# Kernel optimization log

Hardware: AMD Instinct MI355X
Metric: run time of the kernel (lower is better)

The kernel has to match this reference:

```python
import jax, jax.numpy as jnp
import numpy as np
import math

NUM_GROUPS = 32
EPS = 1e-5

def group_norm(x, weight, bias):
    # x: (b, c, h, w); normalize over (c/G, h, w) within each group
    b, c, h, w = x.shape
    xg = x.reshape(b, NUM_GROUPS, c // NUM_GROUPS, h, w)
    mean = xg.mean(axis=(2, 3, 4), keepdims=True)
    var = xg.var(axis=(2, 3, 4), keepdims=True)
    xg = (xg - mean) * jax.lax.rsqrt(var + EPS)
    xn = xg.reshape(b, c, h, w)
    return xn * weight[None, :, None, None] + bias[None, :, None, None]


def setup_inputs() -> dict:
    key = jax.random.key(0)
    ks = jax.random.split(key, 3)
    b, c, h, w = 8, 256, 64, 64
    x = jax.random.normal(ks[0], (b, c, h, w), dtype=jnp.float32)
    gn_weight = jnp.ones((c,), dtype=jnp.float32)
    gn_bias = jnp.zeros((c,), dtype=jnp.float32)
    qkv_w = jax.random.normal(ks[1], (3 * c, c), dtype=jnp.float32) * (1.0 / math.sqrt(c))
    qkv_b = jnp.zeros((3 * c,), dtype=jnp.float32)
    out_w = jax.random.normal(ks[2], (c, c), dtype=jnp.float32) * (1.0 / math.sqrt(c))
    out_b = jnp.zeros((c,), dtype=jnp.float32)
    return {"x": x, "gn_weight": gn_weight, "gn_bias": gn_bias,
            "qkv_w": qkv_w, "qkv_b": qkv_b, "out_w": out_w, "out_b": out_b}


def reference(x, gn_weight, gn_bias, qkv_w, qkv_b, out_w, out_b):
    b, c, h, w = x.shape
    xn = group_norm(x, gn_weight, gn_bias)
    # 1x1 conv == per-pixel matmul: (3c, c) x (b, c, h, w) -> (b, 3c, h, w)
    qkv = jnp.einsum('oc,bchw->bohw', qkv_w, xn) + qkv_b[None, :, None, None]
    q, k, v = jnp.split(qkv, 3, axis=1)
    hw = h * w
    q = q.transpose(0, 2, 3, 1).reshape(b, hw, c)   # (b, hw, c)
    k = k.reshape(b, c, hw)                          # (b, c, hw)
    v = v.transpose(0, 2, 3, 1).reshape(b, hw, c)   # (b, hw, c)
    scale = 1.0 / math.sqrt(c)
    attn = jax.nn.softmax(jnp.einsum('bic,bcj->bij', q, k) * scale, axis=-1)
    out = jnp.einsum('bij,bjc->bic', attn, v)        # (b, hw, c)
    out = out.reshape(b, h, w, c).transpose(0, 3, 1, 2)  # (b, c, h, w)
    out = jnp.einsum('oc,bchw->bohw', out_w, out) + out_b[None, :, None, None]
    return out + x
```

## Files before the change

### kernel.cpp

```cpp
#include <hip/hip_runtime.h>

#define HW 4096
#define NC 256
#define NB 8
#define GN_EPS 1e-5f

typedef short bf16x8 __attribute__((ext_vector_type(8)));
typedef float f32x4 __attribute__((ext_vector_type(4)));
typedef float f32x16 __attribute__((ext_vector_type(16)));

#define MFMA16 __builtin_amdgcn_mfma_f32_16x16x32_bf16
#define MFMA32 __builtin_amdgcn_mfma_f32_32x32x16_bf16

#define SWZ(row) ((((row) & 7) ^ (((row) >> 3) & 7)) << 4)

#define QSCALE 0.09016844f

__device__ __forceinline__ unsigned short f2bf(float f) {
  unsigned int u = __float_as_uint(f);
  u = (u + 0x7FFFu + ((u >> 16) & 1u)) >> 16;
  return (unsigned short)u;
}
__device__ __forceinline__ float bf2f(unsigned short h) {
  return __uint_as_float(((unsigned int)h) << 16);
}

__device__ __forceinline__ void gload16(const void* g, void* l) {
  __builtin_amdgcn_global_load_lds(
      (const __attribute__((address_space(1))) void*)g,
      (__attribute__((address_space(3))) void*)l, 16, 0, 0);
}

__global__ void gn_stats_kernel(const float* __restrict__ x,
                                const float* __restrict__ gnw,
                                const float* __restrict__ gnb,
                                float* __restrict__ s_arr,
                                float* __restrict__ t_arr) {
  int bg = blockIdx.x;
  int b = bg >> 5, g = bg & 31;
  const float4* base = (const float4*)(x + ((size_t)b * NC + g * 8) * HW);
  int tid = threadIdx.x;
  float s = 0.f, ss = 0.f;
  for (int it = 0; it < 32; ++it) {
    float4 v = base[tid + it * 256];
    s += v.x + v.y + v.z + v.w;
    ss += v.x * v.x + v.y * v.y + v.z * v.z + v.w * v.w;
  }
  for (int off = 32; off; off >>= 1) {
    s += __shfl_down(s, off);
    ss += __shfl_down(ss, off);
  }
  __shared__ float red[8];
  __shared__ float bc[2];
  int wave = tid >> 6, lane = tid & 63;
  if (lane == 0) { red[wave] = s; red[4 + wave] = ss; }
  __syncthreads();
  if (tid == 0) {
    float S = red[0] + red[1] + red[2] + red[3];
    float SS = red[4] + red[5] + red[6] + red[7];
    float mean = S * (1.f / 32768.f);
    float var = SS * (1.f / 32768.f) - mean * mean;
    bc[0] = mean;
    bc[1] = rsqrtf(var + GN_EPS);
  }
  __syncthreads();
  if (tid < 8) {
    int c = g * 8 + tid;
    float sv = bc[1] * gnw[c];
    s_arr[b * NC + c] = sv;
    t_arr[b * NC + c] = gnb[c] - bc[0] * sv;
  }
}

__global__ __launch_bounds__(256) void qkv_gemm_kernel(
    const float* __restrict__ x, const float* __restrict__ s_arr,
    const float* __restrict__ t_arr, const float* __restrict__ w,
    const float* __restrict__ bias, unsigned short* __restrict__ qb,
    unsigned short* __restrict__ kc_, unsigned short* __restrict__ vc) {
  int b = blockIdx.z;
  int p0 = blockIdx.x * 64;
  int o0 = blockIdx.y * 128;
  int tid = threadIdx.x;
  int wave = tid >> 6, lane = tid & 63;
  int l15 = lane & 15, q4 = lane >> 4;
  int wm = wave >> 1, wn = wave & 1;
  __shared__ unsigned short a_lds[64 * 64];
  __shared__ unsigned short b_lds[128 * 64];
  char* aB = (char*)a_lds;
  char* bB = (char*)b_lds;
  f32x4 acc[2][4];
  for (int i = 0; i < 2; ++i)
    for (int j = 0; j < 4; ++j) acc[i][j] = (f32x4){0.f, 0.f, 0.f, 0.f};

  for (int kc0 = 0; kc0 < 256; kc0 += 64) {
    __syncthreads();
    for (int it = 0; it < 4; ++it) {
      int idx = tid + it * 256;
      int c = idx >> 4, p4 = idx & 15;
      float4 xv = *(const float4*)(x + ((size_t)b * NC + kc0 + c) * HW + p0 + p4 * 4);
      float sc = s_arr[b * NC + kc0 + c];
      float tc = t_arr[b * NC + kc0 + c];
      float vals[4] = {xv.x, xv.y, xv.z, xv.w};
      for (int i = 0; i < 4; ++i) {
        int p = p4 * 4 + i;
        *(unsigned short*)(aB + ((p * 128 + c * 2) ^ SWZ(p))) =
            f2bf(vals[i] * sc + tc);
      }
    }
    for (int it = 0; it < 8; ++it) {
      int idx = tid + it * 256;
      int o = idx >> 4, c4 = idx & 15;
      float4 wv = *(const float4*)(w + (size_t)(o0 + o) * NC + kc0 + c4 * 4);
      ushort4 hv = make_ushort4(f2bf(wv.x), f2bf(wv.y), f2bf(wv.z), f2bf(wv.w));
      *(ushort4*)(bB + ((o * 128 + c4 * 8) ^ SWZ(o))) = hv;
    }
    __syncthreads();
    for (int kk = 0; kk < 2; ++kk) {
      bf16x8 af[2], bfv[4];
      for (int pb = 0; pb < 2; ++pb) {
        int row = wm * 32 + pb * 16 + l15;
        af[pb] = *(const bf16x8*)(aB + ((row * 128 + kk * 64 + q4 * 16) ^ SWZ(row)));
      }
      for (int ob = 0; ob < 4; ++ob) {
        int row = wn * 64 + ob * 16 + l15;
        bfv[ob] = *(const bf16x8*)(bB + ((row * 128 + kk * 64 + q4 * 16) ^ SWZ(row)));
      }
      for (int pb = 0; pb < 2; ++pb)
        for (int ob = 0; ob < 4; ++ob)
          acc[pb][ob] = MFMA16(af[pb], bfv[ob], acc[pb][ob], 0, 0, 0);
    }
  }
  for (int pb = 0; pb < 2; ++pb) {
    for (int ob = 0; ob < 4; ++ob) {
      int og = o0 + wn * 64 + ob * 16 + l15;
      int tsel = og >> 8, oc = og & 255;
      float bi = bias[og];
      if (tsel == 2) {
        int p = p0 + wm * 32 + pb * 16 + q4 * 4;
        ushort4 pk4 = make_ushort4(
            f2bf(acc[pb][ob][0] + bi), f2bf(acc[pb][ob][1] + bi),
            f2bf(acc[pb][ob][2] + bi), f2bf(acc[pb][ob][3] + bi));
        *(ushort4*)(vc + (((size_t)b * 512 + (p >> 3)) * 256 + oc) * 8 + (p & 7)) =
            pk4;
      } else {
        for (int r = 0; r < 4; ++r) {
          int p = p0 + wm * 32 + pb * 16 + q4 * 4 + r;
          float val = acc[pb][ob][r] + bi;
          if (tsel == 0) {
            qb[((size_t)b * HW + p) * NC + oc] = f2bf(val * QSCALE);
          } else {
            kc_[((size_t)(b * 32 + (oc >> 3)) * HW + p) * 8 + (oc & 7)] = f2bf(val);
          }
        }
      }
    }
  }
}

__global__ __launch_bounds__(256, 2) void flash_attn_kernel(
    const unsigned short* __restrict__ qb, const unsigned short* __restrict__ kc_,
    const unsigned short* __restrict__ vc, unsigned short* __restrict__ Oh0,
    unsigned short* __restrict__ Oh1, float* __restrict__ Lb) {
  int b = blockIdx.x & 7;
  int qt = (blockIdx.x >> 3) & 31;
  int half = blockIdx.x >> 8;
  int tid = threadIdx.x;
  int wave = tid >> 6, lane = tid & 63;
  int l31 = lane & 31;
  int hi = lane >> 5;

  __shared__ unsigned short k_lds[2][8192];
  __shared__ unsigned short v_lds[2][8192];

  int j0b = half * 2048;

  const char* kp[4];
  const char* vp[4];
  {
    const char* kcb = (const char*)(kc_ + (size_t)b * 32 * HW * 8);
    const char* vcb = (const char*)(vc + (size_t)b * 512 * NC * 8);
#pragma unroll
    for (int i = 0; i < 4; ++i) {
      kp[i] = kcb + (size_t)((tid >> 5) + i * 8) * 65536 +
              (size_t)(j0b + (tid & 31)) * 16;
      vp[i] = vcb + (size_t)((j0b >> 3) + i) * 4096 + tid * 16;
    }
  }

  bf16x8 qf[16];
  {
    const unsigned short* qrow =
        qb + ((size_t)b * HW + qt * 128 + wave * 32 + l31) * NC;
#pragma unroll
    for (int kb = 0; kb < 16; ++kb)
      qf[kb] = *(const bf16x8*)(qrow + kb * 16 + hi * 8);
  }

  f32x16 acc[8];
#pragma unroll
  for (int nb = 0; nb < 8; ++nb)
#pragma unroll
    for (int i = 0; i < 16; ++i) acc[nb][i] = 0.f;
  float m_r = -1e30f, l_r = 0.f;

#pragma unroll
  for (int i = 0; i < 4; ++i)
    gload16(kp[i], (char*)k_lds[0] + tid * 16 + i * 4096);
#pragma unroll
  for (int i = 0; i < 4; ++i)
    gload16(vp[i], (char*)v_lds[0] + tid * 16 + i * 4096);
  __syncthreads();

  for (int t = 0; t < 64; ++t) {
    int cur = t & 1;
    if (t < 63) {
#pragma unroll
      for (int i = 0; i < 4; ++i) {
        kp[i] += 512;
        gload16(kp[i], (char*)k_lds[cur ^ 1] + tid * 16 + i * 4096);
      }
#pragma unroll
      for (int i = 0; i < 4; ++i) {
        vp[i] += 16384;
        gload16(vp[i], (char*)v_lds[cur ^ 1] + tid * 16 + i * 4096);
      }
    }
    const char* kB = (const char*)k_lds[cur];
    const char* vB = (const char*)v_lds[cur];

    f32x16 p;
#pragma unroll
    for (int i = 0; i < 16; ++i) p[i] = 0.f;
    __builtin_amdgcn_s_setprio(1);
#pragma unroll
    for (int kb = 0; kb < 16; ++kb) {
      bf16x8 kf = *(const bf16x8*)(kB + (kb * 2 + hi) * 512 + l31 * 16);
      p = MFMA32(kf, qf[kb], p, 0, 0, 0);
    }
    __builtin_amdgcn_s_setprio(0);

    float pmax;
    {
      float t0 = fmaxf(p[0], p[1]), t1 = fmaxf(p[2], p[3]);
      float t2 = fmaxf(p[4], p[5]), t3 = fmaxf(p[6], p[7]);
      float t4 = fmaxf(p[8], p[9]), t5 = fmaxf(p[10], p[11]);
      float t6 = fmaxf(p[12], p[13]), t7 = fmaxf(p[14], p[15]);
      float u0 = fmaxf(t0, t1), u1 = fmaxf(t2, t3);
      float u2 = fmaxf(t4, t5), u3 = fmaxf(t6, t7);
      pmax = fmaxf(fmaxf(u0, u1), fmaxf(u2, u3));
    }
    pmax = fmaxf(pmax, __shfl_xor(pmax, 32));
    if (!__all(pmax - m_r <= 12.0f)) {
      float mn = fmaxf(m_r, pmax);
      float sf = exp2f(m_r - mn);
      m_r = mn;
      l_r *= sf;
#pragma unroll
      for (int reg = 0; reg < 16; ++reg) {
        float sfr = __shfl(sf, (reg & 3) + 8 * (reg >> 2) + 4 * hi);
#pragma unroll
        for (int nb = 0; nb < 8; ++nb) acc[nb][reg] *= sfr;
      }
    }
#pragma unroll
    for (int i = 0; i < 16; ++i) p[i] = __builtin_amdgcn_exp2f(p[i] - m_r);
    float rs;
    {
      float t0 = p[0] + p[1], t1 = p[2] + p[3];
      float t2 = p[4] + p[5], t3 = p[6] + p[7];
      float t4 = p[8] + p[9], t5 = p[10] + p[11];
      float t6 = p[12] + p[13], t7 = p[14] + p[15];
      float u0 = t0 + t1, u1 = t2 + t3, u2 = t4 + t5, u3 = t6 + t7;
      rs = (u0 + u1) + (u2 + u3);
    }
    rs += __shfl_xor(rs, 32);
    l_r += rs;

    int pk[8];
#pragma unroll
    for (int i = 0; i < 8; ++i) {
      int r;
      asm("v_cvt_pk_bf16_f32 %0, %1, %2"
          : "=v"(r)
          : "v"(p[2 * i]), "v"(p[2 * i + 1]));
      pk[i] = r;
    }
    union PU { int w[4]; bf16x8 v; } pu[2];
#pragma unroll
    for (int kb = 0; kb < 2; ++kb) {
      int base = 4 * kb;
      int pushA = hi ? pk[base + 0] : pk[base + 2];
      int pushB = hi ? pk[base + 1] : pk[base + 3];
      int shA = __shfl_xor(pushA, 32);
      int shB = __shfl_xor(pushB, 32);
      pu[kb].w[0] = hi ? shA : pk[base + 0];
      pu[kb].w[1] = hi ? shB : pk[base + 1];
      pu[kb].w[2] = hi ? pk[base + 2] : shA;
      pu[kb].w[3] = hi ? pk[base + 3] : shB;
    }

    __builtin_amdgcn_s_setprio(1);
#pragma unroll
    for (int nb = 0; nb < 8; ++nb) {
#pragma unroll
      for (int kb = 0; kb < 2; ++kb) {
        bf16x8 vf = *(const bf16x8*)(vB + (kb * 2 + hi) * 4096 +
                                     (nb * 32 + l31) * 16);
        acc[nb] = MFMA32(pu[kb].v, vf, acc[nb], 0, 0, 0);
      }
    }
    __builtin_amdgcn_s_setprio(0);
    __syncthreads();
  }

  float linv = 1.f / l_r;
  unsigned short* Ohp = (half ? Oh1 : Oh0) +
                        ((size_t)b * HW + qt * 128 + wave * 32) * NC;
#pragma unroll
  for (int reg = 0; reg < 16; ++reg) {
    int row = (reg & 3) + 8 * (reg >> 2) + 4 * hi;
    float lr = __shfl(linv, row);
#pragma unroll
    for (int nb = 0; nb < 8; ++nb)
      Ohp[(size_t)row * NC + nb * 32 + l31] = f2bf(acc[nb][reg] * lr);
  }
  if (lane < 32) {
    float* Lp = Lb + (size_t)half * NB * HW;
    Lp[(size_t)b * HW + qt * 128 + wave * 32 + lane] = m_r + log2f(l_r);
  }
}

__global__ __launch_bounds__(256) void outproj_kernel(
    const float* __restrict__ ow, const float* __restrict__ obias,
    const unsigned short* __restrict__ Oh0, const unsigned short* __restrict__ Oh1,
    const float* __restrict__ Lb, const float* __restrict__ x,
    float* __restrict__ out) {
  int b = blockIdx.y;
  int p0 = blockIdx.x * 64;
  int tid = threadIdx.x;
  int wave = tid >> 6, lane = tid & 63;
  int l15 = lane & 15, q4 = lane >> 4;
  __shared__ unsigned short aw_lds[256 * 64];
  __shared__ unsigned short bt_lds[64 * 64];
  char* aB = (char*)aw_lds;
  char* bB = (char*)bt_lds;
  f32x4 acc[4][4];
  for (int i = 0; i < 4; ++i)
    for (int j = 0; j < 4; ++j) acc[i][j] = (f32x4){0.f, 0.f, 0.f, 0.f};

  for (int kc0 = 0; kc0 < 256; kc0 += 64) {
    __syncthreads();
    for (int it = 0; it < 16; ++it) {
      int idx = tid + it * 256;
      int o = idx >> 4, c4 = idx & 15;
      float4 wv = *(const float4*)(ow + (size_t)o * NC + kc0 + c4 * 4);
      ushort4 hv = make_ushort4(f2bf(wv.x), f2bf(wv.y), f2bf(wv.z), f2bf(wv.w));
      *(ushort4*)(aB + ((o * 128 + c4 * 8) ^ SWZ(o))) = hv;
    }
    for (int it = 0; it < 2; ++it) {
      int idx = tid + it * 256;
      int p = idx >> 3, c8i = idx & 7;
      int row = p0 + p;
      float L1 = Lb[(size_t)b * HW + row];
      float L2 = Lb[(size_t)(NB + b) * HW + row];
      float w1 = 1.f / (1.f + exp2f(L2 - L1));
      float w2 = 1.f - w1;
      const unsigned short* o1p = Oh0 + ((size_t)b * HW + row) * NC + kc0 + c8i * 8;
      const unsigned short* o2p = Oh1 + ((size_t)b * HW + row) * NC + kc0 + c8i * 8;
      uint4 ra = *(const uint4*)o1p;
      uint4 rb = *(const uint4*)o2p;
      unsigned int aw[4] = {ra.x, ra.y, ra.z, ra.w};
      unsigned int bw[4] = {rb.x, rb.y, rb.z, rb.w};
      unsigned int outw[4];
      for (int i = 0; i < 4; ++i) {
        float lo = w1 * bf2f((unsigned short)(aw[i] & 0xffffu)) +
                   w2 * bf2f((unsigned short)(bw[i] & 0xffffu));
        float hic = w1 * bf2f((unsigned short)(aw[i] >> 16)) +
                    w2 * bf2f((unsigned short)(bw[i] >> 16));
        outw[i] = (unsigned int)f2bf(lo) | ((unsigned int)f2bf(hic) << 16);
      }
      *(uint4*)(bB + ((p * 128 + c8i * 16) ^ SWZ(p))) =
          make_uint4(outw[0], outw[1], outw[2], outw[3]);
    }
    __syncthreads();
    for (int kk = 0; kk < 2; ++kk) {
      bf16x8 af[4], bfv[4];
      for (int obk = 0; obk < 4; ++obk) {
        int row = wave * 64 + obk * 16 + l15;
        af[obk] = *(const bf16x8*)(aB + ((row * 128 + kk * 64 + q4 * 16) ^ SWZ(row)));
      }
      for (int pb = 0; pb < 4; ++pb) {
        int row = pb * 16 + l15;
        bfv[pb] = *(const bf16x8*)(bB + ((row * 128 + kk * 64 + q4 * 16) ^ SWZ(row)));
      }
      for (int obk = 0; obk < 4; ++obk)
        for (int pb = 0; pb < 4; ++pb)
          acc[obk][pb] = MFMA16(af[obk], bfv[pb], acc[obk][pb], 0, 0, 0);
    }
  }
  for (int obk = 0; obk < 4; ++obk)
    for (int pb = 0; pb < 4; ++pb)
      for (int r = 0; r < 4; ++r) {
        int o = wave * 64 + obk * 16 + q4 * 4 + r;
        int p = p0 + pb * 16 + l15;
        size_t gi = ((size_t)b * NC + o) * HW + p;
        out[gi] = acc[obk][pb][r] + obias[o] + x[gi];
      }
}

extern "C" void kernel_launch(void* const* d_in, const int* in_sizes, int n_in,
                              void* d_out, int out_size, void* d_ws, size_t ws_size,
                              hipStream_t stream) {
  (void)in_sizes; (void)n_in; (void)out_size; (void)ws_size;
  const float* x = (const float*)d_in[0];
  const float* gnw = (const float*)d_in[1];
  const float* gnb = (const float*)d_in[2];
  const float* qkvw = (const float*)d_in[3];
  const float* qkvb = (const float*)d_in[4];
  const float* ow = (const float*)d_in[5];
  const float* obias = (const float*)d_in[6];
  float* out = (float*)d_out;

  char* ws = (char*)d_ws;
  float* s_arr = (float*)ws;
  float* t_arr = s_arr + NB * NC;
  size_t tsz = (size_t)NB * HW * NC;
  unsigned short* qb = (unsigned short*)(ws + 16384);
  unsigned short* kc_ = qb + tsz;
  unsigned short* Oh0 = kc_ + tsz;
  unsigned short* vc = Oh0 + tsz;
  unsigned short* Oh1 = vc + tsz;
  float* Lb = (float*)(Oh1 + tsz);

  hipLaunchKernelGGL(gn_stats_kernel, dim3(NB * 32), dim3(256), 0, stream,
                     x, gnw, gnb, s_arr, t_arr);
  hipLaunchKernelGGL(qkv_gemm_kernel, dim3(64, 6, NB), dim3(256), 0, stream,
                     x, s_arr, t_arr, qkvw, qkvb, qb, kc_, vc);
  hipLaunchKernelGGL(flash_attn_kernel, dim3(512), dim3(256), 0, stream,
                     qb, kc_, vc, Oh0, Oh1, Lb);
  hipLaunchKernelGGL(outproj_kernel, dim3(64, NB), dim3(256), 0, stream,
                     ow, obias, Oh0, Oh1, Lb, x, out);
}
```

Before: 239.9 us.

## Precompute bf16 weights and normalized activations, double-buffer QKV GEMM with async loads

Adds a kernel that converts the QKV and output-projection weights to bf16 once per call, and a kernel that applies group norm and writes x transposed to pixel-major bf16. The QKV GEMM then streams bf16 tiles directly into double-buffered LDS with gload16, overlapping the next tile's load with MFMA work. The output projection also loads pre-converted bf16 weights and uses a packed bf16 convert instruction. This removes repeated fp32 loads and per-block conversion, at the cost of two extra launches and a round trip of the normalized activations through global memory (reusing the Oh1 buffer).

```diff
diff --git a/kernel.cpp b/kernel.cpp
--- a/kernel.cpp
+++ b/kernel.cpp
@@ -72,9 +72,55 @@
   }
 }
 
+__global__ void wconv_kernel(const float* __restrict__ qkvw,
+                             const float* __restrict__ ow,
+                             unsigned short* __restrict__ wb) {
+  int i = blockIdx.x * 256 + threadIdx.x;
+  int off = i * 8;
+  const float* src = (i < 24576) ? (qkvw + off) : (ow + (off - 196608));
+  float4 a = *(const float4*)src;
+  float4 c = *(const float4*)(src + 4);
+  *(ushort4*)(wb + off) =
+      make_ushort4(f2bf(a.x), f2bf(a.y), f2bf(a.z), f2bf(a.w));
+  *(ushort4*)(wb + off + 4) =
+      make_ushort4(f2bf(c.x), f2bf(c.y), f2bf(c.z), f2bf(c.w));
+}
+
+__global__ __launch_bounds__(256) void gn_apply_kernel(
+    const float* __restrict__ x, const float* __restrict__ s_arr,
+    const float* __restrict__ t_arr, unsigned short* __restrict__ xt) {
+  int b = blockIdx.z;
+  int p0 = blockIdx.x * 64, c0 = blockIdx.y * 64;
+  int tid = threadIdx.x;
+  __shared__ unsigned short tl[64 * 64];
+  char* tB = (char*)tl;
+  int cl = tid >> 4, p4 = tid & 15;
+#pragma unroll
+  for (int rep = 0; rep < 4; ++rep) {
+    int c = cl + rep * 16;
+    float4 xv = *(const float4*)(x + ((size_t)b * NC + c0 + c) * HW + p0 + p4 * 4);
+    float sc = s_arr[b * NC + c0 + c];
+    float tc = t_arr[b * NC + c0 + c];
+    float vals[4] = {xv.x, xv.y, xv.z, xv.w};
+#pragma unroll
+    for (int i = 0; i < 4; ++i) {
+      int p = p4 * 4 + i;
+      *(unsigned short*)(tB + ((p * 128 + c * 2) ^ SWZ(p))) =
+          f2bf(vals[i] * sc + tc);
+    }
+  }
+  __syncthreads();
+#pragma unroll
+  for (int rep = 0; rep < 2; ++rep) {
+    int p = (tid >> 3) + rep * 32;
+    int c8 = (tid & 7) * 8;
+    bf16x8 v = *(const bf16x8*)(tB + ((p * 128 + c8 * 2) ^ SWZ(p)));
+    *(bf16x8*)(xt + ((size_t)b * HW + p0 + p) * NC + c0 + c8) = v;
+  }
+}
+
 __global__ __launch_bounds__(256) void qkv_gemm_kernel(
-    const float* __restrict__ x, const float* __restrict__ s_arr,
-    const float* __restrict__ t_arr, const float* __restrict__ w,
+    const unsigned short* __restrict__ xt, const unsigned short* __restrict__ wb,
     const float* __restrict__ bias, unsigned short* __restrict__ qb,
     unsigned short* __restrict__ kc_, unsigned short* __restrict__ vc) {
   int b = blockIdx.z;
@@ -84,52 +130,76 @@
   int wave = tid >> 6, lane = tid & 63;
   int l15 = lane & 15, q4 = lane >> 4;
   int wm = wave >> 1, wn = wave & 1;
-  __shared__ unsigned short a_lds[64 * 64];
-  __shared__ unsigned short b_lds[128 * 64];
-  char* aB = (char*)a_lds;
-  char* bB = (char*)b_lds;
+  __shared__ unsigned short a_lds[2][64 * 64];
+  __shared__ unsigned short b_lds[2][128 * 64];
+
+  const char* xtb = (const char*)(xt + ((size_t)b * HW + p0) * NC);
+  const char* wbb = (const char*)wb + o0 * 512;
+  unsigned int asrc[2], bsrc[4];
+#pragma unroll
+  for (int i = 0; i < 2; ++i) {
+    int dk = wave * 2048 + i * 1024 + lane * 16;
+    int row = dk >> 7;
+    asrc[i] = row * 512 + ((dk & 127) ^ SWZ(row));
+  }
+#pragma unroll
+  for (int i = 0; i < 4; ++i) {
+    int dk = wave * 4096 + i * 1024 + lane * 16;
+    int row = dk >> 7;
+    bsrc[i] = row * 512 + ((dk & 127) ^ SWZ(row));
+  }
+
   f32x4 acc[2][4];
+#pragma unroll
   for (int i = 0; i < 2; ++i)
+#pragma unroll
     for (int j = 0; j < 4; ++j) acc[i][j] = (f32x4){0.f, 0.f, 0.f, 0.f};
 
-  for (int kc0 = 0; kc0 < 256; kc0 += 64) {
-    __syncthreads();
-    for (int it = 0; it < 4; ++it) {
-      int idx = tid + it * 256;
-      int c = idx >> 4, p4 = idx & 15;
-      float4 xv = *(const float4*)(x + ((size_t)b * NC + kc0 + c) * HW + p0 + p4 * 4);
-      float sc = s_arr[b * NC + kc0 + c];
-      float tc = t_arr[b * NC + kc0 + c];
-      float vals[4] = {xv.x, xv.y, xv.z, xv.w};
-      for (int i = 0; i < 4; ++i) {
-        int p = p4 * 4 + i;
-        *(unsigned short*)(aB + ((p * 128 + c * 2) ^ SWZ(p))) =
-            f2bf(vals[i] * sc + tc);
-      }
-    }
-    for (int it = 0; it < 8; ++it) {
-      int idx = tid + it * 256;
-      int o = idx >> 4, c4 = idx & 15;
-      float4 wv = *(const float4*)(w + (size_t)(o0 + o) * NC + kc0 + c4 * 4);
-      ushort4 hv = make_ushort4(f2bf(wv.x), f2bf(wv.y), f2bf(wv.z), f2bf(wv.w));
-      *(ushort4*)(bB + ((o * 128 + c4 * 8) ^ SWZ(o))) = hv;
-    }
-    __syncthreads();
+#pragma unroll
+  for (int i = 0; i < 2; ++i)
+    gload16(xtb + asrc[i], (char*)a_lds[0] + wave * 2048 + i * 1024 + lane * 16);
+#pragma unroll
+  for (int i = 0; i < 4; ++i)
+    gload16(wbb + bsrc[i], (char*)b_lds[0] + wave * 4096 + i * 1024 + lane * 16);
+  __syncthreads();
+
+  for (int kc = 0; kc < 4; ++kc) {
+    int cur = kc & 1;
+    if (kc < 3) {
+      int koff = (kc + 1) * 128;
+#pragma unroll
+      for (int i = 0; i < 2; ++i)
+        gload16(xtb + asrc[i] + koff,
+                (char*)a_lds[cur ^ 1] + wave * 2048 + i * 1024 + lane * 16);
+#pragma unroll
+      for (int i = 0; i < 4; ++i)
+        gload16(wbb + bsrc[i] + koff,
+                (char*)b_lds[cur ^ 1] + wave * 4096 + i * 1024 + lane * 16);
+    }
+    const char* aB = (const char*)a_lds[cur];
+    const char* bB = (const char*)b_lds[cur];
+#pragma unroll
     for (int kk = 0; kk < 2; ++kk) {
       bf16x8 af[2], bfv[4];
+#pragma unroll
       for (int pb = 0; pb < 2; ++pb) {
         int row = wm * 32 + pb * 16 + l15;
         af[pb] = *(const bf16x8*)(aB + ((row * 128 + kk * 64 + q4 * 16) ^ SWZ(row)));
       }
+#pragma unroll
       for (int ob = 0; ob < 4; ++ob) {
         int row = wn * 64 + ob * 16 + l15;
         bfv[ob] = *(const bf16x8*)(bB + ((row * 128 + kk * 64 + q4 * 16) ^ SWZ(row)));
       }
+#pragma unroll
       for (int pb = 0; pb < 2; ++pb)
+#pragma unroll
         for (int ob = 0; ob < 4; ++ob)
           acc[pb][ob] = MFMA16(af[pb], bfv[ob], acc[pb][ob], 0, 0, 0);
     }
-  }
+    __syncthreads();
+  }
+
   for (int pb = 0; pb < 2; ++pb) {
     for (int ob = 0; ob < 4; ++ob) {
       int og = o0 + wn * 64 + ob * 16 + l15;
@@ -331,7 +401,7 @@
 }
 
 __global__ __launch_bounds__(256) void outproj_kernel(
-    const float* __restrict__ ow, const float* __restrict__ obias,
+    const unsigned short* __restrict__ owb, const float* __restrict__ obias,
     const unsigned short* __restrict__ Oh0, const unsigned short* __restrict__ Oh1,
     const float* __restrict__ Lb, const float* __restrict__ x,
     float* __restrict__ out) {
@@ -344,19 +414,26 @@
   __shared__ unsigned short bt_lds[64 * 64];
   char* aB = (char*)aw_lds;
   char* bB = (char*)bt_lds;
+
+  unsigned int wsrc[8];
+#pragma unroll
+  for (int i = 0; i < 8; ++i) {
+    int dk = wave * 8192 + i * 1024 + lane * 16;
+    int row = dk >> 7;
+    wsrc[i] = row * 512 + ((dk & 127) ^ SWZ(row));
+  }
+  const char* owbb = (const char*)owb;
+
   f32x4 acc[4][4];
   for (int i = 0; i < 4; ++i)
     for (int j = 0; j < 4; ++j) acc[i][j] = (f32x4){0.f, 0.f, 0.f, 0.f};
 
   for (int kc0 = 0; kc0 < 256; kc0 += 64) {
     __syncthreads();
-    for (int it = 0; it < 16; ++it) {
-      int idx = tid + it * 256;
-      int o = idx >> 4, c4 = idx & 15;
-      float4 wv = *(const float4*)(ow + (size_t)o * NC + kc0 + c4 * 4);
-      ushort4 hv = make_ushort4(f2bf(wv.x), f2bf(wv.y), f2bf(wv.z), f2bf(wv.w));
-      *(ushort4*)(aB + ((o * 128 + c4 * 8) ^ SWZ(o))) = hv;
-    }
+#pragma unroll
+    for (int i = 0; i < 8; ++i)
+      gload16(owbb + wsrc[i] + kc0 * 2,
+              aB + wave * 8192 + i * 1024 + lane * 16);
     for (int it = 0; it < 2; ++it) {
       int idx = tid + it * 256;
       int p = idx >> 3, c8i = idx & 7;
@@ -377,12 +454,15 @@
                    w2 * bf2f((unsigned short)(bw[i] & 0xffffu));
         float hic = w1 * bf2f((unsigned short)(aw[i] >> 16)) +
                     w2 * bf2f((unsigned short)(bw[i] >> 16));
-        outw[i] = (unsigned int)f2bf(lo) | ((unsigned int)f2bf(hic) << 16);
+        int r;
+        asm("v_cvt_pk_bf16_f32 %0, %1, %2" : "=v"(r) : "v"(lo), "v"(hic));
+        outw[i] = (unsigned int)r;
       }
       *(uint4*)(bB + ((p * 128 + c8i * 16) ^ SWZ(p))) =
           make_uint4(outw[0], outw[1], outw[2], outw[3]);
     }
     __syncthreads();
+#pragma unroll
     for (int kk = 0; kk < 2; ++kk) {
       bf16x8 af[4], bfv[4];
       for (int obk = 0; obk < 4; ++obk) {
@@ -430,14 +510,21 @@
   unsigned short* Oh0 = kc_ + tsz;
   unsigned short* vc = Oh0 + tsz;
   unsigned short* Oh1 = vc + tsz;
+  unsigned short* xt = Oh1;
   float* Lb = (float*)(Oh1 + tsz);
+  unsigned short* wb = (unsigned short*)(Lb + 2 * NB * HW);
+  unsigned short* owb = wb + 196608;
 
   hipLaunchKernelGGL(gn_stats_kernel, dim3(NB * 32), dim3(256), 0, stream,
                      x, gnw, gnb, s_arr, t_arr);
+  hipLaunchKernelGGL(wconv_kernel, dim3(128), dim3(256), 0, stream,
+                     qkvw, ow, wb);
+  hipLaunchKernelGGL(gn_apply_kernel, dim3(64, 4, NB), dim3(256), 0, stream,
+                     x, s_arr, t_arr, xt);
   hipLaunchKernelGGL(qkv_gemm_kernel, dim3(64, 6, NB), dim3(256), 0, stream,
-                     x, s_arr, t_arr, qkvw, qkvb, qb, kc_, vc);
+                     xt, wb, qkvb, qb, kc_, vc);
   hipLaunchKernelGGL(flash_attn_kernel, dim3(512), dim3(256), 0, stream,
                      qb, kc_, vc, Oh0, Oh1, Lb);
   hipLaunchKernelGGL(outproj_kernel, dim3(64, NB), dim3(256), 0, stream,
-                     ow, obias, Oh0, Oh1, Lb, x, out);
-}
+                     owb, obias, Oh0, Oh1, Lb, x, out);
+}
```

Result: faster. 208.0 us, median of 2 (-13.3%).
